# Optimization experiments

Measured on AMD Instinct MI355X. Metric: run time of the kernel, lower is better.

Reference implementation:

```python
import jax, jax.numpy as jnp
import numpy as np

B, T = 16, 512          # batch, timesteps
IN = 16                 # input_path_dim
D = 128                 # cde_state_dim
H = 256                 # vf_hidden_dim
L = 136                 # logsig_size = 16 + 16*15/2 (depth-2 log-signature)
O = 32                  # output_path_dim


def _linear_params(key, out_f, in_f):
    kw, kb = jax.random.split(key)
    lim = 1.0 / np.sqrt(in_f)
    W = jax.random.uniform(kw, (out_f, in_f), minval=-lim, maxval=lim, dtype=jnp.float32)
    b = jax.random.uniform(kb, (out_f,), minval=-lim, maxval=lim, dtype=jnp.float32)
    return W, b


def setup_inputs() -> dict:
    key = jax.random.key(0)
    ks = jax.random.split(key, 10)
    x0 = jax.random.normal(ks[0], (B, IN), dtype=jnp.float32)
    # log-signature increments are small; scale down for numerical realism
    logsigs = jax.random.normal(ks[1], (B, T - 1, L), dtype=jnp.float32) * 0.01
    # initial MLP: IN -> H -> H -> D (softplus activations, linear final)
    iw1, ib1 = _linear_params(ks[2], H, IN)
    iw2, ib2 = _linear_params(ks[3], H, H)
    iw3, ib3 = _linear_params(ks[4], D, H)
    # vector-field MLP: D -> H -> H -> D*L (softplus, tanh final)
    fw1, fb1 = _linear_params(ks[5], H, D)
    fw2, fb2 = _linear_params(ks[6], H, H)
    fw3, fb3 = _linear_params(ks[7], D * L, H)
    # readout: D -> O
    rw, rb = _linear_params(ks[8], O, D)
    return dict(x0=x0, logsigs=logsigs,
                iw1=iw1, ib1=ib1, iw2=iw2, ib2=ib2, iw3=iw3, ib3=ib3,
                fw1=fw1, fb1=fb1, fw2=fw2, fb2=fb2, fw3=fw3, fb3=fb3,
                rw=rw, rb=rb)


def reference(x0, logsigs, iw1, ib1, iw2, ib2, iw3, ib3,
              fw1, fb1, fw2, fb2, fw3, fb3, rw, rb):
    sp = jax.nn.softplus
    # initial MLP -> h0: (B, D)
    h0 = sp(x0 @ iw1.T + ib1)
    h0 = sp(h0 @ iw2.T + ib2)
    h0 = h0 @ iw3.T + ib3

    def step(h, logsig_t):
        # vector-field MLP: (B, D) -> (B, D*L), tanh final activation
        z = sp(h @ fw1.T + fb1)
        z = sp(z @ fw2.T + fb2)
        z = jnp.tanh(z @ fw3.T + fb3)
        mat = z.reshape(h.shape[0], D, L)          # (B, D, L)
        h_next = h + jnp.einsum('bdl,bl->bd', mat, logsig_t)
        return h_next, h_next

    # scan over time: xs shape (T-1, B, L)
    _, h_hist = jax.lax.scan(step, h0, jnp.swapaxes(logsigs, 0, 1))
    h_all = jnp.concatenate([h0[None, :, :], h_hist], axis=0)  # (T, B, D)
    out = h_all @ rw.T + rb                                     # (T, B, O)
    return jnp.swapaxes(out, 0, 1)                              # (B, T, O)
```

## Files before the change

kernel.cpp:

```cpp
#include <hip/hip_runtime.h>

namespace {
constexpr int kB = 16, kT = 512, kIN = 16, kD = 128, kH = 256, kL = 136, kO = 32;
constexpr int kSteps = kT - 1;
constexpr int NBLK = 256;
constexpr int NTHR = 512;
constexpr int LH   = 68;
constexpr int NTILE = 5;
constexpr int OFF_FW1 = 0;
constexpr int OFF_FW2 = 36864;
constexpr int OFF_AHI = 110592;
constexpr int OFF_ALO = 119040;
constexpr int OFF_DT  = 127488;
constexpr int OFF_OMS = 132864;
constexpr int OFF_Z1S = 137216;
constexpr int OFF_HB  = 138240;
constexpr int OFF_HINC= 138752;
constexpr int OFF_RED = 139264;
constexpr size_t LDS_BYTES = 139776;
}

typedef __attribute__((ext_vector_type(8))) short short8;
typedef __attribute__((ext_vector_type(4))) float f32x4;

union PK { unsigned long long u; struct { float v; unsigned ep; } s; };

__device__ __forceinline__ float softplusf(float x) {
  return fmaxf(x, 0.0f) + log1pf(expf(-fabsf(x)));
}
__device__ __forceinline__ unsigned short f2bf(float x) {
  unsigned u = __float_as_uint(x);
  return (unsigned short)((u + 0x7FFFu + ((u >> 16) & 1u)) >> 16);
}
__device__ __forceinline__ float bf2f(unsigned short h) {
  return __uint_as_float(((unsigned)h) << 16);
}

__global__ void __launch_bounds__(256)
rde_init(const float* __restrict__ x0,
         const float* __restrict__ iw1, const float* __restrict__ ib1,
         const float* __restrict__ iw2, const float* __restrict__ ib2,
         const float* __restrict__ iw3, const float* __restrict__ ib3,
         float* __restrict__ hist) {
  __shared__ float xs[kIN];
  __shared__ __align__(16) float t1[kH];
  __shared__ __align__(16) float t2[kH];
  const int b = blockIdx.x, tid = threadIdx.x;
  if (tid < kIN) xs[tid] = x0[b*kIN + tid];
  __syncthreads();
  {
    float a = ib1[tid];
#pragma unroll
    for (int i = 0; i < kIN; ++i) a = fmaf(xs[i], iw1[tid*kIN + i], a);
    t1[tid] = softplusf(a);
  }
  __syncthreads();
  {
    const float4* wr = (const float4*)(iw2 + (size_t)tid*kH);
    float a = ib2[tid];
#pragma unroll 8
    for (int q = 0; q < kH/4; ++q) {
      float4 w = wr[q];
      a = fmaf(t1[4*q+0], w.x, a); a = fmaf(t1[4*q+1], w.y, a);
      a = fmaf(t1[4*q+2], w.z, a); a = fmaf(t1[4*q+3], w.w, a);
    }
    t2[tid] = softplusf(a);
  }
  __syncthreads();
  if (tid < kD) {
    const float4* wr = (const float4*)(iw3 + (size_t)tid*kH);
    float a = ib3[tid];
#pragma unroll 8
    for (int q = 0; q < kH/4; ++q) {
      float4 w = wr[q];
      a = fmaf(t2[4*q+0], w.x, a); a = fmaf(t2[4*q+1], w.y, a);
      a = fmaf(t2[4*q+2], w.z, a); a = fmaf(t2[4*q+3], w.w, a);
    }
    hist[(size_t)b*kD + tid] = a;
  }
}

__global__ void __launch_bounds__(NTHR, 2)
rde_scan(const float* __restrict__ lsg,
         const float* __restrict__ fw1, const float* __restrict__ fb1,
         const float* __restrict__ fw2, const float* __restrict__ fb2,
         const float* __restrict__ fw3, const float* __restrict__ fb3,
         float* __restrict__ hist,
         unsigned long long* z1x, unsigned* z2x, unsigned* z2snt,
         unsigned long long* partx) {
  extern __shared__ char smem[];
  float* fw1s = (float*)(smem + OFF_FW1);
  float* fw2s = (float*)(smem + OFF_FW2);
  unsigned short* Ahi = (unsigned short*)(smem + OFF_AHI);
  unsigned short* Alo = (unsigned short*)(smem + OFF_ALO);
  float* Dt   = (float*)(smem + OFF_DT);
  float* oms  = (float*)(smem + OFF_OMS);
  float* z1s  = (float*)(smem + OFF_Z1S);
  float* hb   = (float*)(smem + OFF_HB);
  float* hinc = (float*)(smem + OFF_HINC);
  float* red  = (float*)(smem + OFF_RED);

  const int tid  = threadIdx.x;
  const int k    = blockIdx.x;
  const int wave = tid >> 6, lane = tid & 63;
  const int d_own = k >> 1, l0 = (k & 1) * LH;
  const bool isMLP = (k < 64);
  const int bmlp = k >> 2, qm = k & 3, j0 = qm * 64;
  const int jj = tid >> 3, ks = tid & 7;

  short8 bhi[8], blo[8];
  float biasv = 0.f;
  {
#pragma unroll
    for (int s = 0; s < 8; ++s) { bhi[s] = (short8)0; blo[s] = (short8)0; }
    if (wave < NTILE) {
      const int nl = wave*16 + (lane & 15);
      const int g  = lane >> 4;
      if (nl < LH) {
        const size_t row = (size_t)d_own*kL + l0 + nl;
        const float* wrow = fw3 + row*kH;
        biasv = fb3[row];
#pragma unroll
        for (int s = 0; s < 8; ++s) {
          const int k0 = s*32 + g*8;
          float4 v0 = *(const float4*)(wrow + k0);
          float4 v1 = *(const float4*)(wrow + k0 + 4);
          float vv[8] = {v0.x,v0.y,v0.z,v0.w,v1.x,v1.y,v1.z,v1.w};
#pragma unroll
          for (int e = 0; e < 8; ++e) {
            unsigned short hh = f2bf(vv[e]);
            bhi[s][e] = (short)hh;
            blo[s][e] = (short)f2bf(vv[e] - bf2f(hh));
          }
        }
      }
    }
  }
  float myfb1 = 0.f, myfb2 = 0.f;
  if (isMLP) {
    myfb1 = fb1[j0 + jj]; myfb2 = fb2[j0 + jj];
    for (int i = tid; i < 64*32; i += NTHR) {
      int j = i >> 5, q = i & 31;
      float4 v = *(const float4*)(fw1 + (size_t)(j0 + j)*kD + q*4);
      *(float2*)(fw1s + (2*q  )*144 + 2*j) = make_float2(v.x, v.y);
      *(float2*)(fw1s + (2*q+1)*144 + 2*j) = make_float2(v.z, v.w);
    }
    for (int i = tid; i < 64*64; i += NTHR) {
      int j = i >> 6, q = i & 63;
      float4 v = *(const float4*)(fw2 + (size_t)(j0 + j)*kH + q*4);
      *(float2*)(fw2s + (2*q  )*144 + 2*j) = make_float2(v.x, v.y);
      *(float2*)(fw2s + (2*q+1)*144 + 2*j) = make_float2(v.z, v.w);
    }
    for (int i = tid; i < kD; i += NTHR) hb[i] = hist[(size_t)bmlp*kD + i];
  }
  __syncthreads();

  for (int t = 0; t < kSteps; ++t) {
    const unsigned epw = (unsigned)(t + 1);

    if (!isMLP) {
      if (tid >= 256) {
        int c = tid - 256;
#pragma unroll 2
        for (int rep = 0; rep < 2; ++rep) {
          int cc = c + rep*256;
          if (cc < 272) {
            int bb = cc / 17, ii = cc % 17;
            float4 v = *(const float4*)(lsg + ((size_t)bb*kSteps + t)*kL + l0 + ii*4);
            *(float4*)(oms + bb*LH + ii*4) = v;
          }
        }
      }
    } else {
      {
        float a = 0.f;
#pragma unroll
        for (int kh = ks; kh < 64; kh += 8) {
          float2 w  = *(const float2*)(fw1s + kh*144 + 2*jj);
          float2 h2 = *(const float2*)(hb + 2*kh);
          a = fmaf(h2.x, w.x, a); a = fmaf(h2.y, w.y, a);
        }
        a += __shfl_xor(a, 1); a += __shfl_xor(a, 2); a += __shfl_xor(a, 4);
        if (ks == 0) {
          PK p; p.s.v = softplusf(a + myfb1); p.s.ep = epw;
          __hip_atomic_store(z1x + bmlp*kH + j0 + jj, p.u,
                             __ATOMIC_RELAXED, __HIP_MEMORY_SCOPE_AGENT);
        }
      }
      if (tid >= 256) {
        int c = tid - 256;
#pragma unroll 2
        for (int rep = 0; rep < 2; ++rep) {
          int cc = c + rep*256;
          if (cc < 272) {
            int bb = cc / 17, ii = cc % 17;
            float4 v = *(const float4*)(lsg + ((size_t)bb*kSteps + t)*kL + l0 + ii*4);
            *(float4*)(oms + bb*LH + ii*4) = v;
          }
        }
      }
      if (tid < 128) {
#pragma unroll
        for (int s = 0; s < 2; ++s) {
          int idx = tid*2 + s;
          PK q;
          for (;;) {
            q.u = __hip_atomic_load(z1x + bmlp*kH + idx,
                                    __ATOMIC_RELAXED, __HIP_MEMORY_SCOPE_AGENT);
            if (q.s.ep == epw) break;
            __builtin_amdgcn_s_sleep(1);
          }
          z1s[idx] = q.s.v;
        }
      }
      __syncthreads();
      asm volatile("" ::: "memory");
      {
        float a = 0.f;
#pragma unroll
        for (int kh = ks; kh < 128; kh += 8) {
          float2 w  = *(const float2*)(fw2s + kh*144 + 2*jj);
          float2 z2v = *(const float2*)(z1s + 2*kh);
          a = fmaf(z2v.x, w.x, a); a = fmaf(z2v.y, w.y, a);
        }
        a += __shfl_xor(a, 1); a += __shfl_xor(a, 2); a += __shfl_xor(a, 4);
        if (ks == 0) {
          float v = softplusf(a + myfb2);
          unsigned short hh = f2bf(v);
          unsigned short ll = f2bf(v - bf2f(hh));
          __hip_atomic_store(z2x + bmlp*kH + j0 + jj,
                             (unsigned)hh | ((unsigned)ll << 16),
                             __ATOMIC_RELAXED, __HIP_MEMORY_SCOPE_AGENT);
        }
      }
      __syncthreads();
      if (tid == 0)
        __hip_atomic_store(z2snt + (bmlp*4 + qm)*32, epw,
                           __ATOMIC_RELAXED, __HIP_MEMORY_SCOPE_AGENT);
    }

    if (tid < 64) {
      for (;;) {
        unsigned e = __hip_atomic_load(z2snt + tid*32,
                                       __ATOMIC_RELAXED, __HIP_MEMORY_SCOPE_AGENT);
        if (e == epw) break;
        __builtin_amdgcn_s_sleep(2);
      }
    }
    __syncthreads();
    asm volatile("" ::: "memory");
    {
      unsigned pk[8];
      const unsigned* src = z2x + tid*8;
#pragma unroll
      for (int i = 0; i < 8; ++i)
        pk[i] = __hip_atomic_load(src + i, __ATOMIC_RELAXED, __HIP_MEMORY_SCOPE_AGENT);
      const int e0 = tid*8, m = e0 >> 8, kk = e0 & 255;
      unsigned short* ph = Ahi + m*264 + kk;
      unsigned short* pl = Alo + m*264 + kk;
#pragma unroll
      for (int i = 0; i < 4; ++i) {
        unsigned a = pk[2*i], b = pk[2*i+1];
        *(unsigned*)(ph + 2*i) = (a & 0xffffu) | (b << 16);
        *(unsigned*)(pl + 2*i) = (a >> 16) | (b & 0xffff0000u);
      }
    }
    __syncthreads();

    if (wave < NTILE) {
      f32x4 acc = {biasv, biasv, biasv, biasv};
      const unsigned short* arh = Ahi + (lane & 15)*264;
      const unsigned short* arl = Alo + (lane & 15)*264;
      const int g = lane >> 4;
#pragma unroll
      for (int s = 0; s < 8; ++s) {
        short8 ah = *(const short8*)(arh + s*32 + g*8);
        short8 al = *(const short8*)(arl + s*32 + g*8);
        acc = __builtin_amdgcn_mfma_f32_16x16x32_bf16(ah, bhi[s], acc, 0, 0, 0);
        acc = __builtin_amdgcn_mfma_f32_16x16x32_bf16(ah, blo[s], acc, 0, 0, 0);
        acc = __builtin_amdgcn_mfma_f32_16x16x32_bf16(al, bhi[s], acc, 0, 0, 0);
      }
#pragma unroll
      for (int r = 0; r < 4; ++r)
        Dt[(g*4 + r)*84 + wave*16 + (lane & 15)] = acc[r];
    }
    __syncthreads();

    {
      const int b3 = tid & 15, lb = tid >> 4;
      float p = tanhf(Dt[b3*84 + lb     ]) * oms[b3*LH + lb     ]
              + tanhf(Dt[b3*84 + lb + 32]) * oms[b3*LH + lb + 32];
      if (lb < 4)
        p += tanhf(Dt[b3*84 + lb + 64]) * oms[b3*LH + lb + 64];
      p += __shfl_xor(p, 16); p += __shfl_xor(p, 32);
      if (lane < 16) red[lane*8 + wave] = p;
    }
    __syncthreads();
    if (tid < 16) {
      float s = 0.f;
#pragma unroll
      for (int j = 0; j < 8; ++j) s += red[tid*8 + j];
      PK p; p.s.v = s; p.s.ep = epw;
      __hip_atomic_store(partx + tid*NBLK + k, p.u,
                         __ATOMIC_RELAXED, __HIP_MEMORY_SCOPE_AGENT);
    }

    if (isMLP) {
      float pval = 0.f;
      if (tid < 256) {
        PK q;
        for (;;) {
          q.u = __hip_atomic_load(partx + bmlp*NBLK + tid,
                                  __ATOMIC_RELAXED, __HIP_MEMORY_SCOPE_AGENT);
          if (q.s.ep == epw) break;
          __builtin_amdgcn_s_sleep(2);
        }
        pval = q.s.v;
        float p2 = pval + __shfl_xor(pval, 1);
        if ((tid & 1) == 0) hinc[tid >> 1] = p2;
      }
      __syncthreads();
      if (tid < 128) {
        float hn = hb[tid] + hinc[tid];
        hb[tid] = hn;
        if (qm == 0) hist[((size_t)(t+1)*kB + bmlp)*kD + tid] = hn;
      }
      __syncthreads();
    }
  }
}

__global__ void __launch_bounds__(512)
rde_readout(const float* __restrict__ hist, const float* __restrict__ rw,
            const float* __restrict__ rb, float* __restrict__ out) {
  const int t = blockIdx.x, tid = threadIdx.x;
  const int b = tid >> 5, o = tid & 31;
  const float4* hr = (const float4*)(hist + ((size_t)t*kB + b)*kD);
  const float4* wr = (const float4*)(rw + (size_t)o*kD);
  float a = rb[o];
#pragma unroll 8
  for (int q = 0; q < kD/4; ++q) {
    float4 h4 = hr[q], w4 = wr[q];
    a = fmaf(h4.x,w4.x,a); a = fmaf(h4.y,w4.y,a);
    a = fmaf(h4.z,w4.z,a); a = fmaf(h4.w,w4.w,a);
  }
  out[((size_t)b*kT + t)*kO + o] = a;
}

extern "C" void kernel_launch(void* const* d_in, const int* in_sizes, int n_in,
                              void* d_out, int out_size, void* d_ws, size_t ws_size,
                              hipStream_t stream) {
  const float* x0  = (const float*)d_in[0];
  const float* lsg = (const float*)d_in[1];
  const float* iw1 = (const float*)d_in[2];
  const float* ib1 = (const float*)d_in[3];
  const float* iw2 = (const float*)d_in[4];
  const float* ib2 = (const float*)d_in[5];
  const float* iw3 = (const float*)d_in[6];
  const float* ib3 = (const float*)d_in[7];
  const float* fw1 = (const float*)d_in[8];
  const float* fb1 = (const float*)d_in[9];
  const float* fw2 = (const float*)d_in[10];
  const float* fb2 = (const float*)d_in[11];
  const float* fw3 = (const float*)d_in[12];
  const float* fb3 = (const float*)d_in[13];
  const float* rw  = (const float*)d_in[14];
  const float* rb  = (const float*)d_in[15];
  float* out = (float*)d_out;

  float* hist = (float*)d_ws;
  unsigned long long* z1x = (unsigned long long*)(hist + (size_t)kT*kB*kD);
  unsigned* z2x   = (unsigned*)(z1x + kB*kH);
  unsigned* z2snt = z2x + kB*kH;
  unsigned long long* partx = (unsigned long long*)(z2snt + 64*32);

  size_t xbytes = (size_t)kB*kH*8 + (size_t)kB*kH*4 + 64*32*4 + (size_t)kB*NBLK*8;
  hipMemsetAsync(z1x, 0, xbytes, stream);
  hipFuncSetAttribute((const void*)rde_scan,
                      hipFuncAttributeMaxDynamicSharedMemorySize, (int)LDS_BYTES);

  rde_init<<<kB, 256, 0, stream>>>(x0, iw1, ib1, iw2, ib2, iw3, ib3, hist);

  void* args[] = { (void*)&lsg, (void*)&fw1, (void*)&fb1, (void*)&fw2, (void*)&fb2,
                   (void*)&fw3, (void*)&fb3, (void*)&hist, (void*)&z1x, (void*)&z2x,
                   (void*)&z2snt, (void*)&partx };
  hipLaunchCooperativeKernel((const void*)rde_scan, dim3(NBLK), dim3(NTHR),
                             args, (unsigned)LDS_BYTES, stream);

  rde_readout<<<kT, 512, 0, stream>>>(hist, rw, rb, out);
}
```

Measured before the change: 4.777 ms.

## Give each batch row one MLP block and move fw3 bf16 tiles into LDS

The first two vector-field layers are no longer split across four blocks per batch row. One block per row now computes both layers with fw1/fw2 held in registers, which removes the cross-block z1 exchange and one grid-level wait per step. The z2 handoff now tags each 64-bit element with the step number, so consumers poll the data directly instead of a separate sentinel array. The fw3 hi/lo bf16 split moves from registers into LDS. The costs are heavy register pressure (192 floats per thread) and more serial MLP work per block.

```diff
diff --git a/kernel.cpp b/kernel.cpp
--- a/kernel.cpp
+++ b/kernel.cpp
@@ -7,23 +7,20 @@
 constexpr int NTHR = 512;
 constexpr int LH   = 68;
 constexpr int NTILE = 5;
-constexpr int OFF_FW1 = 0;
-constexpr int OFF_FW2 = 36864;
-constexpr int OFF_AHI = 110592;
-constexpr int OFF_ALO = 119040;
-constexpr int OFF_DT  = 127488;
-constexpr int OFF_OMS = 132864;
-constexpr int OFF_Z1S = 137216;
-constexpr int OFF_HB  = 138240;
-constexpr int OFF_HINC= 138752;
-constexpr int OFF_RED = 139264;
-constexpr size_t LDS_BYTES = 139776;
+constexpr int OFF_W3L = 0;
+constexpr int OFF_AHI = 81920;
+constexpr int OFF_ALO = 90368;
+constexpr int OFF_DT  = 98816;
+constexpr int OFF_OMS = 104192;
+constexpr int OFF_Z1S = 108544;
+constexpr int OFF_HB  = 109568;
+constexpr int OFF_HINC= 110080;
+constexpr int OFF_RED = 110592;
+constexpr size_t LDS_BYTES = 111104;
 }
 
 typedef __attribute__((ext_vector_type(8))) short short8;
 typedef __attribute__((ext_vector_type(4))) float f32x4;
-
-union PK { unsigned long long u; struct { float v; unsigned ep; } s; };
 
 __device__ __forceinline__ float softplusf(float x) {
   return fmaxf(x, 0.0f) + log1pf(expf(-fabsf(x)));
@@ -35,6 +32,8 @@
 __device__ __forceinline__ float bf2f(unsigned short h) {
   return __uint_as_float(((unsigned)h) << 16);
 }
+#define ALOAD64(p)   __hip_atomic_load((p),  __ATOMIC_RELAXED, __HIP_MEMORY_SCOPE_AGENT)
+#define ASTORE64(p,v) __hip_atomic_store((p), (v), __ATOMIC_RELAXED, __HIP_MEMORY_SCOPE_AGENT)
 
 __global__ void __launch_bounds__(256)
 rde_init(const float* __restrict__ x0,
@@ -86,11 +85,9 @@
          const float* __restrict__ fw2, const float* __restrict__ fb2,
          const float* __restrict__ fw3, const float* __restrict__ fb3,
          float* __restrict__ hist,
-         unsigned long long* z1x, unsigned* z2x, unsigned* z2snt,
-         unsigned long long* partx) {
+         unsigned long long* z2x, unsigned long long* partx) {
   extern __shared__ char smem[];
-  float* fw1s = (float*)(smem + OFF_FW1);
-  float* fw2s = (float*)(smem + OFF_FW2);
+  unsigned short* W3L = (unsigned short*)(smem + OFF_W3L);
   unsigned short* Ahi = (unsigned short*)(smem + OFF_AHI);
   unsigned short* Alo = (unsigned short*)(smem + OFF_ALO);
   float* Dt   = (float*)(smem + OFF_DT);
@@ -104,163 +101,124 @@
   const int k    = blockIdx.x;
   const int wave = tid >> 6, lane = tid & 63;
   const int d_own = k >> 1, l0 = (k & 1) * LH;
-  const bool isMLP = (k < 64);
-  const int bmlp = k >> 2, qm = k & 3, j0 = qm * 64;
-  const int jj = tid >> 3, ks = tid & 7;
-
-  short8 bhi[8], blo[8];
+  const bool isMLP = (k < kB);
+  const int b_own = k;
+  const int j = tid >> 1, ksp = tid & 1;
+
+  for (int i = tid; i < NTILE*8*64; i += NTHR) {
+    const int w = i >> 9, s = (i >> 6) & 7, ln = i & 63;
+    const int nl = w*16 + (ln & 15), g = ln >> 4;
+    unsigned hi4[4], lo4[4];
+    if (nl < LH) {
+      const float* wrow = fw3 + ((size_t)d_own*kL + l0 + nl)*kH + s*32 + g*8;
+#pragma unroll
+      for (int e = 0; e < 4; ++e) {
+        float v0 = wrow[2*e], v1 = wrow[2*e+1];
+        unsigned short h0 = f2bf(v0), h1 = f2bf(v1);
+        unsigned short l0_ = f2bf(v0 - bf2f(h0)), l1_ = f2bf(v1 - bf2f(h1));
+        hi4[e] = (unsigned)h0 | ((unsigned)h1 << 16);
+        lo4[e] = (unsigned)l0_ | ((unsigned)l1_ << 16);
+      }
+    } else {
+#pragma unroll
+      for (int e = 0; e < 4; ++e) { hi4[e] = 0u; lo4[e] = 0u; }
+    }
+    unsigned* dh = (unsigned*)(W3L + (((w*8+s)*2+0)*64 + ln)*8);
+    unsigned* dl = (unsigned*)(W3L + (((w*8+s)*2+1)*64 + ln)*8);
+#pragma unroll
+    for (int e = 0; e < 4; ++e) { dh[e] = hi4[e]; dl[e] = lo4[e]; }
+  }
   float biasv = 0.f;
-  {
-#pragma unroll
-    for (int s = 0; s < 8; ++s) { bhi[s] = (short8)0; blo[s] = (short8)0; }
-    if (wave < NTILE) {
-      const int nl = wave*16 + (lane & 15);
-      const int g  = lane >> 4;
-      if (nl < LH) {
-        const size_t row = (size_t)d_own*kL + l0 + nl;
-        const float* wrow = fw3 + row*kH;
-        biasv = fb3[row];
-#pragma unroll
-        for (int s = 0; s < 8; ++s) {
-          const int k0 = s*32 + g*8;
-          float4 v0 = *(const float4*)(wrow + k0);
-          float4 v1 = *(const float4*)(wrow + k0 + 4);
-          float vv[8] = {v0.x,v0.y,v0.z,v0.w,v1.x,v1.y,v1.z,v1.w};
-#pragma unroll
-          for (int e = 0; e < 8; ++e) {
-            unsigned short hh = f2bf(vv[e]);
-            bhi[s][e] = (short)hh;
-            blo[s][e] = (short)f2bf(vv[e] - bf2f(hh));
-          }
-        }
-      }
-    }
-  }
+  if (wave < NTILE) {
+    int nl = wave*16 + (lane & 15);
+    if (nl < LH) biasv = fb3[(size_t)d_own*kL + l0 + nl];
+  }
+  float w1r[64], w2r[128];
   float myfb1 = 0.f, myfb2 = 0.f;
   if (isMLP) {
-    myfb1 = fb1[j0 + jj]; myfb2 = fb2[j0 + jj];
-    for (int i = tid; i < 64*32; i += NTHR) {
-      int j = i >> 5, q = i & 31;
-      float4 v = *(const float4*)(fw1 + (size_t)(j0 + j)*kD + q*4);
-      *(float2*)(fw1s + (2*q  )*144 + 2*j) = make_float2(v.x, v.y);
-      *(float2*)(fw1s + (2*q+1)*144 + 2*j) = make_float2(v.z, v.w);
-    }
-    for (int i = tid; i < 64*64; i += NTHR) {
-      int j = i >> 6, q = i & 63;
-      float4 v = *(const float4*)(fw2 + (size_t)(j0 + j)*kH + q*4);
-      *(float2*)(fw2s + (2*q  )*144 + 2*j) = make_float2(v.x, v.y);
-      *(float2*)(fw2s + (2*q+1)*144 + 2*j) = make_float2(v.z, v.w);
-    }
-    for (int i = tid; i < kD; i += NTHR) hb[i] = hist[(size_t)bmlp*kD + i];
+    const float* p1 = fw1 + (size_t)j*kD + ksp*64;
+#pragma unroll
+    for (int q = 0; q < 16; ++q) {
+      float4 v = *(const float4*)(p1 + 4*q);
+      w1r[4*q] = v.x; w1r[4*q+1] = v.y; w1r[4*q+2] = v.z; w1r[4*q+3] = v.w;
+    }
+    const float* p2 = fw2 + (size_t)j*kH + ksp*128;
+#pragma unroll
+    for (int q = 0; q < 32; ++q) {
+      float4 v = *(const float4*)(p2 + 4*q);
+      w2r[4*q] = v.x; w2r[4*q+1] = v.y; w2r[4*q+2] = v.z; w2r[4*q+3] = v.w;
+    }
+    myfb1 = fb1[j]; myfb2 = fb2[j];
+    for (int i = tid; i < kD; i += NTHR) hb[i] = hist[(size_t)b_own*kD + i];
   }
   __syncthreads();
 
   for (int t = 0; t < kSteps; ++t) {
     const unsigned epw = (unsigned)(t + 1);
 
-    if (!isMLP) {
-      if (tid >= 256) {
-        int c = tid - 256;
-#pragma unroll 2
-        for (int rep = 0; rep < 2; ++rep) {
-          int cc = c + rep*256;
-          if (cc < 272) {
-            int bb = cc / 17, ii = cc % 17;
-            float4 v = *(const float4*)(lsg + ((size_t)bb*kSteps + t)*kL + l0 + ii*4);
-            *(float4*)(oms + bb*LH + ii*4) = v;
-          }
-        }
-      }
-    } else {
+    if (isMLP) {
       {
         float a = 0.f;
 #pragma unroll
-        for (int kh = ks; kh < 64; kh += 8) {
-          float2 w  = *(const float2*)(fw1s + kh*144 + 2*jj);
-          float2 h2 = *(const float2*)(hb + 2*kh);
-          a = fmaf(h2.x, w.x, a); a = fmaf(h2.y, w.y, a);
-        }
-        a += __shfl_xor(a, 1); a += __shfl_xor(a, 2); a += __shfl_xor(a, 4);
-        if (ks == 0) {
-          PK p; p.s.v = softplusf(a + myfb1); p.s.ep = epw;
-          __hip_atomic_store(z1x + bmlp*kH + j0 + jj, p.u,
-                             __ATOMIC_RELAXED, __HIP_MEMORY_SCOPE_AGENT);
-        }
-      }
-      if (tid >= 256) {
-        int c = tid - 256;
+        for (int q = 0; q < 16; ++q) {
+          float4 h4 = *(const float4*)(hb + ksp*64 + 4*q);
+          a = fmaf(h4.x, w1r[4*q  ], a); a = fmaf(h4.y, w1r[4*q+1], a);
+          a = fmaf(h4.z, w1r[4*q+2], a); a = fmaf(h4.w, w1r[4*q+3], a);
+        }
+        a += __shfl_xor(a, 1);
+        if (ksp == 0) z1s[j] = softplusf(a + myfb1);
+      }
+      __syncthreads();
+      {
+        float c = 0.f;
+#pragma unroll
+        for (int q = 0; q < 32; ++q) {
+          float4 z4 = *(const float4*)(z1s + ksp*128 + 4*q);
+          c = fmaf(z4.x, w2r[4*q  ], c); c = fmaf(z4.y, w2r[4*q+1], c);
+          c = fmaf(z4.z, w2r[4*q+2], c); c = fmaf(z4.w, w2r[4*q+3], c);
+        }
+        c += __shfl_xor(c, 1);
+        if (ksp == 0) {
+          float v = softplusf(c + myfb2);
+          unsigned short hh = f2bf(v), ll = f2bf(v - bf2f(hh));
+          unsigned long long pk = (unsigned long long)((unsigned)hh | ((unsigned)ll << 16))
+                                | ((unsigned long long)epw << 32);
+          ASTORE64(z2x + b_own*kH + j, pk);
+        }
+      }
+    }
+
+    if (tid >= 256) {
+      int c = tid - 256;
 #pragma unroll 2
-        for (int rep = 0; rep < 2; ++rep) {
-          int cc = c + rep*256;
-          if (cc < 272) {
-            int bb = cc / 17, ii = cc % 17;
-            float4 v = *(const float4*)(lsg + ((size_t)bb*kSteps + t)*kL + l0 + ii*4);
-            *(float4*)(oms + bb*LH + ii*4) = v;
-          }
-        }
-      }
-      if (tid < 128) {
-#pragma unroll
-        for (int s = 0; s < 2; ++s) {
-          int idx = tid*2 + s;
-          PK q;
-          for (;;) {
-            q.u = __hip_atomic_load(z1x + bmlp*kH + idx,
-                                    __ATOMIC_RELAXED, __HIP_MEMORY_SCOPE_AGENT);
-            if (q.s.ep == epw) break;
-            __builtin_amdgcn_s_sleep(1);
-          }
-          z1s[idx] = q.s.v;
-        }
-      }
-      __syncthreads();
-      asm volatile("" ::: "memory");
-      {
-        float a = 0.f;
-#pragma unroll
-        for (int kh = ks; kh < 128; kh += 8) {
-          float2 w  = *(const float2*)(fw2s + kh*144 + 2*jj);
-          float2 z2v = *(const float2*)(z1s + 2*kh);
-          a = fmaf(z2v.x, w.x, a); a = fmaf(z2v.y, w.y, a);
-        }
-        a += __shfl_xor(a, 1); a += __shfl_xor(a, 2); a += __shfl_xor(a, 4);
-        if (ks == 0) {
-          float v = softplusf(a + myfb2);
-          unsigned short hh = f2bf(v);
-          unsigned short ll = f2bf(v - bf2f(hh));
-          __hip_atomic_store(z2x + bmlp*kH + j0 + jj,
-                             (unsigned)hh | ((unsigned)ll << 16),
-                             __ATOMIC_RELAXED, __HIP_MEMORY_SCOPE_AGENT);
-        }
-      }
-      __syncthreads();
-      if (tid == 0)
-        __hip_atomic_store(z2snt + (bmlp*4 + qm)*32, epw,
-                           __ATOMIC_RELAXED, __HIP_MEMORY_SCOPE_AGENT);
-    }
-
-    if (tid < 64) {
+      for (int rep = 0; rep < 2; ++rep) {
+        int cc = c + rep*256;
+        if (cc < 272) {
+          int bb = cc / 17, ii = cc % 17;
+          float4 v = *(const float4*)(lsg + ((size_t)bb*kSteps + t)*kL + l0 + ii*4);
+          *(float4*)(oms + bb*LH + ii*4) = v;
+        }
+      }
+    }
+
+    {
+      const unsigned long long* src = z2x + tid*8;
+      unsigned long long q8[8];
       for (;;) {
-        unsigned e = __hip_atomic_load(z2snt + tid*32,
-                                       __ATOMIC_RELAXED, __HIP_MEMORY_SCOPE_AGENT);
-        if (e == epw) break;
-        __builtin_amdgcn_s_sleep(2);
-      }
-    }
-    __syncthreads();
-    asm volatile("" ::: "memory");
-    {
-      unsigned pk[8];
-      const unsigned* src = z2x + tid*8;
-#pragma unroll
-      for (int i = 0; i < 8; ++i)
-        pk[i] = __hip_atomic_load(src + i, __ATOMIC_RELAXED, __HIP_MEMORY_SCOPE_AGENT);
+        bool ok = true;
+#pragma unroll
+        for (int i = 0; i < 8; ++i) q8[i] = ALOAD64(src + i);
+#pragma unroll
+        for (int i = 0; i < 8; ++i) ok &= ((unsigned)(q8[i] >> 32) == epw);
+        if (ok) break;
+        __builtin_amdgcn_s_sleep(1);
+      }
       const int e0 = tid*8, m = e0 >> 8, kk = e0 & 255;
       unsigned short* ph = Ahi + m*264 + kk;
       unsigned short* pl = Alo + m*264 + kk;
 #pragma unroll
       for (int i = 0; i < 4; ++i) {
-        unsigned a = pk[2*i], b = pk[2*i+1];
+        unsigned a = (unsigned)q8[2*i], b = (unsigned)q8[2*i+1];
         *(unsigned*)(ph + 2*i) = (a & 0xffffu) | (b << 16);
         *(unsigned*)(pl + 2*i) = (a >> 16) | (b & 0xffff0000u);
       }
@@ -269,20 +227,22 @@
 
     if (wave < NTILE) {
       f32x4 acc = {biasv, biasv, biasv, biasv};
-      const unsigned short* arh = Ahi + (lane & 15)*264;
-      const unsigned short* arl = Alo + (lane & 15)*264;
-      const int g = lane >> 4;
+      const int l15 = lane & 15, g = lane >> 4;
+      const unsigned short* arh = Ahi + l15*264;
+      const unsigned short* arl = Alo + l15*264;
 #pragma unroll
       for (int s = 0; s < 8; ++s) {
         short8 ah = *(const short8*)(arh + s*32 + g*8);
         short8 al = *(const short8*)(arl + s*32 + g*8);
-        acc = __builtin_amdgcn_mfma_f32_16x16x32_bf16(ah, bhi[s], acc, 0, 0, 0);
-        acc = __builtin_amdgcn_mfma_f32_16x16x32_bf16(ah, blo[s], acc, 0, 0, 0);
-        acc = __builtin_amdgcn_mfma_f32_16x16x32_bf16(al, bhi[s], acc, 0, 0, 0);
+        short8 bh = *(const short8*)(W3L + ((wave*16 + s*2 + 0)*64 + lane)*8);
+        short8 bl = *(const short8*)(W3L + ((wave*16 + s*2 + 1)*64 + lane)*8);
+        acc = __builtin_amdgcn_mfma_f32_16x16x32_bf16(ah, bh, acc, 0, 0, 0);
+        acc = __builtin_amdgcn_mfma_f32_16x16x32_bf16(ah, bl, acc, 0, 0, 0);
+        acc = __builtin_amdgcn_mfma_f32_16x16x32_bf16(al, bh, acc, 0, 0, 0);
       }
 #pragma unroll
       for (int r = 0; r < 4; ++r)
-        Dt[(g*4 + r)*84 + wave*16 + (lane & 15)] = acc[r];
+        Dt[(g*4 + r)*84 + wave*16 + l15] = acc[r];
     }
     __syncthreads();
 
@@ -299,31 +259,30 @@
     if (tid < 16) {
       float s = 0.f;
 #pragma unroll
-      for (int j = 0; j < 8; ++j) s += red[tid*8 + j];
-      PK p; p.s.v = s; p.s.ep = epw;
-      __hip_atomic_store(partx + tid*NBLK + k, p.u,
-                         __ATOMIC_RELAXED, __HIP_MEMORY_SCOPE_AGENT);
+      for (int jw = 0; jw < 8; ++jw) s += red[tid*8 + jw];
+      unsigned long long pk = (unsigned long long)__float_as_uint(s)
+                            | ((unsigned long long)epw << 32);
+      ASTORE64(partx + tid*NBLK + k, pk);
     }
 
     if (isMLP) {
-      float pval = 0.f;
       if (tid < 256) {
-        PK q;
+        const unsigned long long* pp = partx + b_own*NBLK + tid;
+        unsigned long long q;
         for (;;) {
-          q.u = __hip_atomic_load(partx + bmlp*NBLK + tid,
-                                  __ATOMIC_RELAXED, __HIP_MEMORY_SCOPE_AGENT);
-          if (q.s.ep == epw) break;
-          __builtin_amdgcn_s_sleep(2);
-        }
-        pval = q.s.v;
-        float p2 = pval + __shfl_xor(pval, 1);
+          q = ALOAD64(pp);
+          if ((unsigned)(q >> 32) == epw) break;
+          __builtin_amdgcn_s_sleep(1);
+        }
+        float pv = __uint_as_float((unsigned)q);
+        float p2 = pv + __shfl_xor(pv, 1);
         if ((tid & 1) == 0) hinc[tid >> 1] = p2;
       }
       __syncthreads();
       if (tid < 128) {
         float hn = hb[tid] + hinc[tid];
         hb[tid] = hn;
-        if (qm == 0) hist[((size_t)(t+1)*kB + bmlp)*kD + tid] = hn;
+        hist[((size_t)(t+1)*kB + b_own)*kD + tid] = hn;
       }
       __syncthreads();
     }
@@ -369,21 +328,17 @@
   float* out = (float*)d_out;
 
   float* hist = (float*)d_ws;
-  unsigned long long* z1x = (unsigned long long*)(hist + (size_t)kT*kB*kD);
-  unsigned* z2x   = (unsigned*)(z1x + kB*kH);
-  unsigned* z2snt = z2x + kB*kH;
-  unsigned long long* partx = (unsigned long long*)(z2snt + 64*32);
-
-  size_t xbytes = (size_t)kB*kH*8 + (size_t)kB*kH*4 + 64*32*4 + (size_t)kB*NBLK*8;
-  hipMemsetAsync(z1x, 0, xbytes, stream);
+  unsigned long long* z2x   = (unsigned long long*)(hist + (size_t)kT*kB*kD);
+  unsigned long long* partx = z2x + (size_t)kB*kH;
+
+  hipMemsetAsync(z2x, 0, (size_t)kB*kH*8 * 2, stream);
   hipFuncSetAttribute((const void*)rde_scan,
                       hipFuncAttributeMaxDynamicSharedMemorySize, (int)LDS_BYTES);
 
   rde_init<<<kB, 256, 0, stream>>>(x0, iw1, ib1, iw2, ib2, iw3, ib3, hist);
 
   void* args[] = { (void*)&lsg, (void*)&fw1, (void*)&fb1, (void*)&fw2, (void*)&fb2,
-                   (void*)&fw3, (void*)&fb3, (void*)&hist, (void*)&z1x, (void*)&z2x,
-                   (void*)&z2snt, (void*)&partx };
+                   (void*)&fw3, (void*)&fb3, (void*)&hist, (void*)&z2x, (void*)&partx };
   hipLaunchCooperativeKernel((const void*)rde_scan, dim3(NBLK), dim3(NTHR),
                              args, (unsigned)LDS_BYTES, stream);
 
```

New measurement: 5.623 ms. +17.7%, slower.
